# Kernel tuning notes

Measured on AMD Instinct MI355X. Metric: run time of the kernel, lower is better.

## Reference

```python
import jax, jax.numpy as jnp
import numpy as np

# Production-scale dims (see shape_source)
B, D_MODEL, L = 2, 1024, 8192
NUM_GROUPS = 256          # d_model of ExplicitSingleDecayFilter
L_CACHE = 128             # explicit filter length (padded to L inside fftconv)
LOG_R_MIN, LOG_R_MAX = 0.0, 2.0  # decay_preset='strong'


def setup_inputs() -> dict:
    key = jax.random.key(0)
    k1, k2, k3, k4, k5 = jax.random.split(key, 5)
    x1 = jax.random.normal(k1, (B, D_MODEL, L), jnp.float32)
    x2 = jax.random.normal(k2, (B, D_MODEL, L), jnp.float32)
    v = jax.random.normal(k3, (B, D_MODEL, L), jnp.float32)
    # h init: randn(d_model, L_cache)/sqrt(L_cache) (small_init scale omitted for numerics)
    h = jax.random.normal(k4, (NUM_GROUPS, L_CACHE), jnp.float32) / np.sqrt(L_CACHE).astype(np.float32)
    conv_bias = jax.random.normal(k5, (D_MODEL,), jnp.float32)
    return {"x1": x1, "x2": x2, "v": v, "h": h, "conv_bias": conv_bias}


def _decay_filter(h):
    # ExplicitSingleDecayFilter: k = h * exp(-logspace(r_min, r_max)[:, None] * linspace(0, 1, L_cache)[None])
    G, Lc = h.shape
    t = jnp.linspace(0.0, 1.0, Lc, dtype=h.dtype)[None]                 # [1, Lc]
    decay_domain = jnp.logspace(LOG_R_MIN, LOG_R_MAX, G, dtype=h.dtype)[:, None]  # [G, 1]
    return h * jnp.exp(-decay_domain * t)                               # [G, Lc]


def reference(x1, x2, v, h, conv_bias):
    Bv, D, Lseq = x1.shape
    G = h.shape[0]
    gd = D // G
    fft_size = 2 * Lseq

    # grouped causal FFT convolution of the gated signal z = x2 * v
    z = (x2 * v).reshape(Bv, G, gd, Lseq)
    x1g = x1.reshape(Bv, G, gd, Lseq)

    k = _decay_filter(h)                                    # [G, L_cache]
    k = jnp.pad(k, ((0, 0), (0, Lseq - k.shape[-1])))       # pad filter to seqlen
    # torch: k_f = rfft(k, n)/n ; y = irfft(u_f*k_f, n, norm='forward')[..., :L]
    # which equals numpy-default irfft(rfft(u, n) * rfft(k, n), n)[..., :L]
    k_f = jnp.fft.rfft(k, n=fft_size)                       # [G, L+1] complex
    z_f = jnp.fft.rfft(z, n=fft_size)                       # [B, G, gd, L+1]
    y = jnp.fft.irfft(z_f * k_f[None, :, None, :], n=fft_size)[..., :Lseq]

    # D shortcut term (conv_bias), no gelu, no dropout in this operator
    Dterm = conv_bias.reshape(G, gd)
    out = y + z * Dterm[None, :, :, None]

    # post-gating by x1, back to [B, D, L] then [B, L, D]
    out = (out * x1g).reshape(Bv, D, Lseq)
    return jnp.transpose(out, (0, 2, 1))
```

## Files before the change

### kernel.cpp

```cpp
#include <hip/hip_runtime.h>

typedef float f4  __attribute__((ext_vector_type(4)));
typedef short s8v __attribute__((ext_vector_type(8)));
typedef short s4v __attribute__((ext_vector_type(4)));

#define BB    2
#define DDIM  1024
#define LSEQ  8192
#define LC    128
#define TD    16
#define TL    512
#define HALO  128
#define ZSTR  648
#define KSTR  176
#define KOFF  16
#define OB2   (TL/8)

__device__ __forceinline__ unsigned bf16pk(float lo, float hi) {
    unsigned a = __float_as_uint(lo), b = __float_as_uint(hi);
    a = (a + 0x7FFFu + ((a >> 16) & 1u)) >> 16;
    b = (b + 0x7FFFu + ((b >> 16) & 1u));
    return (a & 0xFFFFu) | (b & 0xFFFF0000u);
}
__device__ __forceinline__ float bf2f(short s) {
    return __uint_as_float(((unsigned)(unsigned short)s) << 16);
}

union U8 { s8v s; unsigned u[4]; };

__global__ __launch_bounds__(256, 4) void hyena_mfma_kernel(
    const float* __restrict__ x1,
    const float* __restrict__ x2,
    const float* __restrict__ v,
    const float* __restrict__ h,
    const float* __restrict__ cb,
    float* __restrict__ out)
{
    __shared__ union SM {
        struct { short zb[TD][ZSTR]; float kl[4][KSTR]; } s1;
        f4 ob[TD][OB2];
    } sm;

    const int t = threadIdx.x;

    const int flat = blockIdx.x;
    const int xcd  = flat & 7;
    const int rr_  = flat >> 3;
    const int d0   = (rr_ & 63) * TD;
    const int c_   = xcd + 8*(rr_ >> 6);
    const int l0   = (c_ & 15) * TL;
    const int b    = c_ >> 4;

    const int r = t & 15, sbase = t >> 4;
    const size_t rb = ((size_t)(b*DDIM + d0 + r)) * LSEQ;
    f4 xa0[5], xa1[5], xw0[5], xw1[5];
    #pragma unroll
    for (int it = 0; it < 5; ++it) {
        const int gl = l0 - HALO + (sbase + 16*it)*8;
        if (gl >= 0) {
            xa0[it] = *(const f4*)(x2 + rb + gl);
            xa1[it] = *(const f4*)(x2 + rb + gl + 4);
            xw0[it] = *(const f4*)(v  + rb + gl);
            xw1[it] = *(const f4*)(v  + rb + gl + 4);
        }
    }

    for (int idx = t; idx < 4*KSTR; idx += 256) {
        const int gl2 = idx / KSTR, mi = idx - gl2*KSTR;
        const int m  = mi - KOFF;
        float val = 0.f;
        if (m >= 0 && m < LC) {
            const int g = (d0 >> 2) + gl2;
            const float dd = __expf((float)g * (2.0f/255.0f) * 2.302585092994046f);
            val = h[g*LC + m] * __expf(-dd * (float)m * (1.0f/127.0f));
        }
        sm.s1.kl[gl2][mi] = val;
    }

    #pragma unroll
    for (int it = 0; it < 5; ++it) {
        const int s = sbase + 16*it;
        const int gl = l0 - HALO + s*8;
        U8 zz; zz.s = (s8v){0,0,0,0,0,0,0,0};
        if (gl >= 0) {
            const f4 z0 = xa0[it]*xw0[it], z1 = xa1[it]*xw1[it];
            zz.u[0] = bf16pk(z0[0], z0[1]);
            zz.u[1] = bf16pk(z0[2], z0[3]);
            zz.u[2] = bf16pk(z1[0], z1[1]);
            zz.u[3] = bf16pk(z1[2], z1[3]);
        }
        *(s8v*)&sm.s1.zb[r][s*8] = zz.s;
    }

    const int wv = t >> 6, lane = t & 63;
    const int j  = lane & 15, kb = lane >> 4;
    const int qj = j & 3,  cc = j >> 2;
    const int row = wv*4 + cc;
    const size_t chb = ((size_t)(b*DDIM + d0 + row)) * LSEQ + l0;
    f4 x1r[8];
    #pragma unroll
    for (int ci = 0; ci < 8; ++ci)
        x1r[ci] = *(const f4*)(x1 + chb + 64*ci + 16*qj + 4*kb);
    const float bd = cb[d0 + row];
    __syncthreads();

    s8v afr[5];
    #pragma unroll
    for (int u = 0; u < 5; ++u) {
        const int M0 = j - 8*kb + 16 + 32*u;
        float kv[8];
        #pragma unroll
        for (int e = 0; e < 8; ++e) kv[e] = sm.s1.kl[wv][M0 - e + KOFF];
        U8 aa;
        aa.u[0] = bf16pk(kv[0], kv[1]);
        aa.u[1] = bf16pk(kv[2], kv[3]);
        aa.u[2] = bf16pk(kv[4], kv[5]);
        aa.u[3] = bf16pk(kv[6], kv[7]);
        afr[u] = aa.s;
    }

    f4 ov[8];
    #pragma unroll
    for (int ci = 0; ci < 8; ++ci) {
        const int L = 64*ci + 16*qj;
        f4 acc = {0.f, 0.f, 0.f, 0.f};
        #pragma unroll
        for (int u = 0; u < 5; ++u) {
            int bi = 112 + L + 8*kb - 32*u;
            bi = bi < 0 ? 0 : bi;
            const s8v bf = *(const s8v*)&sm.s1.zb[row][bi];
            acc = __builtin_amdgcn_mfma_f32_16x16x32_bf16(afr[u], bf, acc, 0, 0, 0);
        }
        const int lo = L + 4*kb;
        const s4v z4 = *(const s4v*)&sm.s1.zb[row][HALO + lo];
        f4 o;
        o[0] = (acc[0] + bf2f(z4[0])*bd) * x1r[ci][0];
        o[1] = (acc[1] + bf2f(z4[1])*bd) * x1r[ci][1];
        o[2] = (acc[2] + bf2f(z4[2])*bd) * x1r[ci][2];
        o[3] = (acc[3] + bf2f(z4[3])*bd) * x1r[ci][3];
        ov[ci] = o;
    }

    const int seg = t & 3;
    #pragma unroll
    for (int hp = 0; hp < 2; ++hp) {
        __syncthreads();
        #pragma unroll
        for (int ci = 0; ci < 4; ++ci) {
            const int cidx = hp*4 + ci;
            const int J = (4*cidx + qj)*4 + kb - hp*64;
            sm.ob[row][J ^ (row & 7)] = ov[cidx];
        }
        __syncthreads();
        #pragma unroll
        for (int it = 0; it < 4; ++it) {
            const int ll = (t >> 2) + it*64;
            const int J = ll >> 2, e = ll & 3;
            f4 o;
            #pragma unroll
            for (int rr2 = 0; rr2 < 4; ++rr2) {
                const int r2 = seg*4 + rr2;
                o[rr2] = ((const float*)&sm.ob[r2][J ^ (r2 & 7)])[e];
            }
            *(f4*)(out + ((size_t)b*LSEQ + l0 + hp*256 + ll)*DDIM + d0 + seg*4) = o;
        }
    }
}

extern "C" void kernel_launch(void* const* d_in, const int* in_sizes, int n_in,
                              void* d_out, int out_size, void* d_ws, size_t ws_size,
                              hipStream_t stream) {
    const float* x1 = (const float*)d_in[0];
    const float* x2 = (const float*)d_in[1];
    const float* v  = (const float*)d_in[2];
    const float* h  = (const float*)d_in[3];
    const float* cb = (const float*)d_in[4];
    float* outp = (float*)d_out;
    hipLaunchKernelGGL(hyena_mfma_kernel, dim3(2048), dim3(256), 0, stream,
                       x1, x2, v, h, cb, outp);
}
```

Before: 51.17 us.

## Loop four sequence tiles per block with double-buffered z staging

Each block now processes four consecutive 512-element sequence tiles instead of one, so the grid shrinks from 2048 to 512 blocks. The gated z signal is double-buffered in LDS, and the next tile's loads are spread across the current tile's MFMA and store phases. The 128-element halo is reused from the previous tile's buffer rather than reloaded, which removes the redundant halo traffic and repeated filter setup per tile. In exchange there are more barriers per block, higher register pressure (launch bounds lowered to 3), and fewer blocks to spread across the CUs.

```diff
diff --git a/kernel.cpp b/kernel.cpp
--- a/kernel.cpp
+++ b/kernel.cpp
@@ -9,12 +9,13 @@
 #define LSEQ  8192
 #define LC    128
 #define TD    16
-#define TL    512
-#define HALO  128
-#define ZSTR  648
+#define TILE  512
+#define NT    4
+#define SPAN  (TILE*NT)
+#define ZW2   520
 #define KSTR  176
 #define KOFF  16
-#define OB2   (TL/8)
+#define OB2   64
 
 __device__ __forceinline__ unsigned bf16pk(float lo, float hi) {
     unsigned a = __float_as_uint(lo), b = __float_as_uint(hi);
@@ -28,7 +29,17 @@
 
 union U8 { s8v s; unsigned u[4]; };
 
-__global__ __launch_bounds__(256, 4) void hyena_mfma_kernel(
+__device__ __forceinline__ s8v cvt8(const f4& a0, const f4& a1, const f4& w0, const f4& w1) {
+    const f4 z0 = a0*w0, z1 = a1*w1;
+    U8 zz;
+    zz.u[0] = bf16pk(z0[0], z0[1]);
+    zz.u[1] = bf16pk(z0[2], z0[3]);
+    zz.u[2] = bf16pk(z1[0], z1[1]);
+    zz.u[3] = bf16pk(z1[2], z1[3]);
+    return zz.s;
+}
+
+__global__ __launch_bounds__(256, 3) void hyena_pipe_kernel(
     const float* __restrict__ x1,
     const float* __restrict__ x2,
     const float* __restrict__ v,
@@ -36,33 +47,38 @@
     const float* __restrict__ cb,
     float* __restrict__ out)
 {
-    __shared__ union SM {
-        struct { short zb[TD][ZSTR]; float kl[4][KSTR]; } s1;
-        f4 ob[TD][OB2];
-    } sm;
+    __shared__ short zb[2][TD][ZW2];
+    __shared__ float kl[4][KSTR];
+    __shared__ f4    ob[TD][OB2];
 
     const int t = threadIdx.x;
 
     const int flat = blockIdx.x;
     const int xcd  = flat & 7;
-    const int rr_  = flat >> 3;
-    const int d0   = (rr_ & 63) * TD;
-    const int c_   = xcd + 8*(rr_ >> 6);
-    const int l0   = (c_ & 15) * TL;
-    const int b    = c_ >> 4;
+    const int d0   = (flat >> 3) * TD;
+    const int lg   = xcd & 3;
+    const int b    = xcd >> 2;
+    const int bl0  = lg * SPAN;
 
     const int r = t & 15, sbase = t >> 4;
     const size_t rb = ((size_t)(b*DDIM + d0 + r)) * LSEQ;
-    f4 xa0[5], xa1[5], xw0[5], xw1[5];
+
+    f4 pa0[4], pa1[4], pw0[4], pw1[4];
     #pragma unroll
-    for (int it = 0; it < 5; ++it) {
-        const int gl = l0 - HALO + (sbase + 16*it)*8;
-        if (gl >= 0) {
-            xa0[it] = *(const f4*)(x2 + rb + gl);
-            xa1[it] = *(const f4*)(x2 + rb + gl + 4);
-            xw0[it] = *(const f4*)(v  + rb + gl);
-            xw1[it] = *(const f4*)(v  + rb + gl + 4);
-        }
+    for (int it = 0; it < 4; ++it) {
+        const int gl = bl0 + (sbase + 16*it)*8;
+        pa0[it] = *(const f4*)(x2 + rb + gl);
+        pa1[it] = *(const f4*)(x2 + rb + gl + 4);
+        pw0[it] = *(const f4*)(v  + rb + gl);
+        pw1[it] = *(const f4*)(v  + rb + gl + 4);
+    }
+    const int hgl = bl0 - 128 + sbase*8;
+    f4 ha0 = {0,0,0,0}, ha1 = ha0, hw0 = ha0, hw1 = ha0;
+    if (hgl >= 0) {
+        ha0 = *(const f4*)(x2 + rb + hgl);
+        ha1 = *(const f4*)(x2 + rb + hgl + 4);
+        hw0 = *(const f4*)(v  + rb + hgl);
+        hw1 = *(const f4*)(v  + rb + hgl + 4);
     }
 
     for (int idx = t; idx < 4*KSTR; idx += 256) {
@@ -74,34 +90,22 @@
             const float dd = __expf((float)g * (2.0f/255.0f) * 2.302585092994046f);
             val = h[g*LC + m] * __expf(-dd * (float)m * (1.0f/127.0f));
         }
-        sm.s1.kl[gl2][mi] = val;
+        kl[gl2][mi] = val;
     }
 
     #pragma unroll
-    for (int it = 0; it < 5; ++it) {
-        const int s = sbase + 16*it;
-        const int gl = l0 - HALO + s*8;
-        U8 zz; zz.s = (s8v){0,0,0,0,0,0,0,0};
-        if (gl >= 0) {
-            const f4 z0 = xa0[it]*xw0[it], z1 = xa1[it]*xw1[it];
-            zz.u[0] = bf16pk(z0[0], z0[1]);
-            zz.u[1] = bf16pk(z0[2], z0[3]);
-            zz.u[2] = bf16pk(z1[0], z1[1]);
-            zz.u[3] = bf16pk(z1[2], z1[3]);
-        }
-        *(s8v*)&sm.s1.zb[r][s*8] = zz.s;
-    }
+    for (int it = 0; it < 4; ++it)
+        *(s8v*)&zb[0][r][(sbase + 16*it)*8] = cvt8(pa0[it], pa1[it], pw0[it], pw1[it]);
+    { s8v hz = (hgl >= 0) ? cvt8(ha0, ha1, hw0, hw1) : (s8v){0,0,0,0,0,0,0,0};
+      *(s8v*)&zb[1][r][384 + sbase*8] = hz; }
 
     const int wv = t >> 6, lane = t & 63;
     const int j  = lane & 15, kb = lane >> 4;
     const int qj = j & 3,  cc = j >> 2;
     const int row = wv*4 + cc;
-    const size_t chb = ((size_t)(b*DDIM + d0 + row)) * LSEQ + l0;
-    f4 x1r[8];
-    #pragma unroll
-    for (int ci = 0; ci < 8; ++ci)
-        x1r[ci] = *(const f4*)(x1 + chb + 64*ci + 16*qj + 4*kb);
     const float bd = cb[d0 + row];
+    const size_t chbase = ((size_t)(b*DDIM + d0 + row)) * LSEQ + bl0;
+    const int seg = t & 3;
     __syncthreads();
 
     s8v afr[5];
@@ -110,7 +114,7 @@
         const int M0 = j - 8*kb + 16 + 32*u;
         float kv[8];
         #pragma unroll
-        for (int e = 0; e < 8; ++e) kv[e] = sm.s1.kl[wv][M0 - e + KOFF];
+        for (int e = 0; e < 8; ++e) kv[e] = kl[wv][M0 - e + KOFF];
         U8 aa;
         aa.u[0] = bf16pk(kv[0], kv[1]);
         aa.u[1] = bf16pk(kv[2], kv[3]);
@@ -119,39 +123,84 @@
         afr[u] = aa.s;
     }
 
-    f4 ov[8];
-    #pragma unroll
-    for (int ci = 0; ci < 8; ++ci) {
-        const int L = 64*ci + 16*qj;
-        f4 acc = {0.f, 0.f, 0.f, 0.f};
-        #pragma unroll
-        for (int u = 0; u < 5; ++u) {
-            int bi = 112 + L + 8*kb - 32*u;
-            bi = bi < 0 ? 0 : bi;
-            const s8v bf = *(const s8v*)&sm.s1.zb[row][bi];
-            acc = __builtin_amdgcn_mfma_f32_16x16x32_bf16(afr[u], bf, acc, 0, 0, 0);
-        }
-        const int lo = L + 4*kb;
-        const s4v z4 = *(const s4v*)&sm.s1.zb[row][HALO + lo];
-        f4 o;
-        o[0] = (acc[0] + bf2f(z4[0])*bd) * x1r[ci][0];
-        o[1] = (acc[1] + bf2f(z4[1])*bd) * x1r[ci][1];
-        o[2] = (acc[2] + bf2f(z4[2])*bd) * x1r[ci][2];
-        o[3] = (acc[3] + bf2f(z4[3])*bd) * x1r[ci][3];
-        ov[ci] = o;
-    }
-
-    const int seg = t & 3;
-    #pragma unroll
-    for (int hp = 0; hp < 2; ++hp) {
-        __syncthreads();
+    for (int tt = 0; tt < NT; ++tt) {
+        short (*cur)[ZW2] = zb[tt & 1];
+        short (*prv)[ZW2] = zb[(tt + 1) & 1];
+        const bool stage = (tt + 1 < NT);
+        const int tl0 = bl0 + (tt + 1)*TILE;
+
+        f4 sa0[2], sa1[2], sw0[2], sw1[2];
+        if (stage) {
+            #pragma unroll
+            for (int it = 0; it < 2; ++it) {
+                const int gl = tl0 + (sbase + 16*it)*8;
+                sa0[it] = *(const f4*)(x2 + rb + gl);
+                sa1[it] = *(const f4*)(x2 + rb + gl + 4);
+                sw0[it] = *(const f4*)(v  + rb + gl);
+                sw1[it] = *(const f4*)(v  + rb + gl + 4);
+            }
+        }
+
+        const size_t chb = chbase + (size_t)tt*TILE;
+        f4 x1a[4], x1b[4];
+        #pragma unroll
+        for (int ci = 0; ci < 4; ++ci)
+            x1a[ci] = *(const f4*)(x1 + chb + 64*ci + 16*qj + 4*kb);
+        f4 ov[8];
+        #pragma unroll
+        for (int ci = 0; ci < 8; ++ci) {
+            if (ci == 4) {
+                #pragma unroll
+                for (int c2 = 0; c2 < 4; ++c2)
+                    x1b[c2] = *(const f4*)(x1 + chb + 64*(c2+4) + 16*qj + 4*kb);
+            }
+            const int qb = 64*ci + 16*qj + 8*kb - 16;
+            f4 acc = {0.f, 0.f, 0.f, 0.f};
+            #pragma unroll
+            for (int u = 0; u < 5; ++u) {
+                const int q = qb - 32*u;
+                const short* p = (q >= 0) ? &cur[row][q]
+                                          : &prv[row][512 + (q < -128 ? -128 : q)];
+                const s8v bf = *(const s8v*)p;
+                acc = __builtin_amdgcn_mfma_f32_16x16x32_bf16(afr[u], bf, acc, 0, 0, 0);
+            }
+            const int lo = 64*ci + 16*qj + 4*kb;
+            const s4v z4 = *(const s4v*)&cur[row][lo];
+            const f4 xv = (ci < 4) ? x1a[ci] : x1b[ci-4];
+            f4 o;
+            o[0] = (acc[0] + bf2f(z4[0])*bd) * xv[0];
+            o[1] = (acc[1] + bf2f(z4[1])*bd) * xv[1];
+            o[2] = (acc[2] + bf2f(z4[2])*bd) * xv[2];
+            o[3] = (acc[3] + bf2f(z4[3])*bd) * xv[3];
+            ov[ci] = o;
+        }
+
+        f4 ta0[2], ta1[2], tw0[2], tw1[2];
+        if (stage) {
+            #pragma unroll
+            for (int it = 0; it < 2; ++it) {
+                const int gl = tl0 + (sbase + 16*(it+2))*8;
+                ta0[it] = *(const f4*)(x2 + rb + gl);
+                ta1[it] = *(const f4*)(x2 + rb + gl + 4);
+                tw0[it] = *(const f4*)(v  + rb + gl);
+                tw1[it] = *(const f4*)(v  + rb + gl + 4);
+            }
+        }
+
+        __syncthreads();
+
+        if (stage) {
+            #pragma unroll
+            for (int it = 0; it < 2; ++it)
+                *(s8v*)&prv[r][(sbase + 16*it)*8] = cvt8(sa0[it], sa1[it], sw0[it], sw1[it]);
+        }
         #pragma unroll
         for (int ci = 0; ci < 4; ++ci) {
-            const int cidx = hp*4 + ci;
-            const int J = (4*cidx + qj)*4 + kb - hp*64;
-            sm.ob[row][J ^ (row & 7)] = ov[cidx];
-        }
-        __syncthreads();
+            const int J = (4*ci + qj)*4 + kb;
+            ob[row][J ^ (row & 7)] = ov[ci];
+        }
+        __syncthreads();
+
         #pragma unroll
         for (int it = 0; it < 4; ++it) {
             const int ll = (t >> 2) + it*64;
@@ -160,9 +209,35 @@
             #pragma unroll
             for (int rr2 = 0; rr2 < 4; ++rr2) {
                 const int r2 = seg*4 + rr2;
-                o[rr2] = ((const float*)&sm.ob[r2][J ^ (r2 & 7)])[e];
-            }
-            *(f4*)(out + ((size_t)b*LSEQ + l0 + hp*256 + ll)*DDIM + d0 + seg*4) = o;
+                o[rr2] = ((const float*)&ob[r2][J ^ (r2 & 7)])[e];
+            }
+            *(f4*)(out + ((size_t)b*LSEQ + bl0 + tt*TILE + ll)*DDIM + d0 + seg*4) = o;
+        }
+        if (stage) {
+            #pragma unroll
+            for (int it = 0; it < 2; ++it)
+                *(s8v*)&prv[r][(sbase + 16*(it+2))*8] = cvt8(ta0[it], ta1[it], tw0[it], tw1[it]);
+        }
+        __syncthreads();
+
+        #pragma unroll
+        for (int ci = 4; ci < 8; ++ci) {
+            const int J = (4*ci + qj)*4 + kb - 64;
+            ob[row][J ^ (row & 7)] = ov[ci];
+        }
+        __syncthreads();
+
+        #pragma unroll
+        for (int it = 0; it < 4; ++it) {
+            const int ll = (t >> 2) + it*64;
+            const int J = ll >> 2, e = ll & 3;
+            f4 o;
+            #pragma unroll
+            for (int rr2 = 0; rr2 < 4; ++rr2) {
+                const int r2 = seg*4 + rr2;
+                o[rr2] = ((const float*)&ob[r2][J ^ (r2 & 7)])[e];
+            }
+            *(f4*)(out + ((size_t)b*LSEQ + bl0 + tt*TILE + 256 + ll)*DDIM + d0 + seg*4) = o;
         }
     }
 }
@@ -176,6 +251,6 @@
     const float* h  = (const float*)d_in[3];
     const float* cb = (const float*)d_in[4];
     float* outp = (float*)d_out;
-    hipLaunchKernelGGL(hyena_mfma_kernel, dim3(2048), dim3(256), 0, stream,
+    hipLaunchKernelGGL(hyena_pipe_kernel, dim3(512), dim3(256), 0, stream,
                        x1, x2, v, h, cb, outp);
 }
```

New measurement: 69.41 us. +35.6%, slower.
